# Optimization experiments

Hardware: AMD Instinct MI355X
Metric: run time of the kernel (lower is better)

Reference implementation:

```python
import jax, jax.numpy as jnp
import numpy as np

B, N, C, K = 8, 4096, 128, 16
POOL_RATE = 4  # npoint = N // POOL_RATE


def setup_inputs() -> dict:
    key = jax.random.key(0)
    k1, k2, k3 = jax.random.split(key, 3)
    vertices = jax.random.normal(k1, (B, 3, N), dtype=jnp.float32)
    feature_map = jax.random.normal(k2, (B, C, N), dtype=jnp.float32)
    # pre-flattened global knn indices, values in [0, B*N) as produced upstream
    idx = jax.random.randint(k3, (B * N * K,), 0, B * N, dtype=jnp.int64)
    return {"vertices": vertices, "feature_map": feature_map, "idx": idx}


def farthest_point_sample(xyz, npoint):
    """xyz: (B, N, 3) -> centroid indices (B, npoint).
    Deterministic start at index 0 (torch version uses a random start)."""
    b, n, _ = xyz.shape

    def step(carry, _):
        distance, farthest = carry
        centroid = jnp.take_along_axis(xyz, farthest[:, None, None], axis=1)  # (B,1,3)
        dist = jnp.sum((xyz - centroid) ** 2, axis=-1)  # (B,N)
        distance = jnp.minimum(distance, dist)
        new_farthest = jnp.argmax(distance, axis=-1)
        return (distance, new_farthest), farthest

    dist0 = jnp.full((b, n), 1e10, dtype=xyz.dtype)
    far0 = jnp.zeros((b,), dtype=jnp.int32)
    _, cents = jax.lax.scan(step, (dist0, far0), None, length=npoint)
    return cents.T  # (B, npoint)


def reference(vertices, feature_map, idx):
    b, c, n = feature_map.shape
    # get_graph_feature with precomputed flat idx: gather neighbors then max-pool
    flat = feature_map.transpose(0, 2, 1).reshape(b * n, c)        # (B*N, C)
    neigh = flat[idx].reshape(b, n, K, c)                          # (B,N,K,C)
    pooled = jnp.max(neigh, axis=2)                                # (B,N,C) == (B,C,N) pooled_feature, channel-last

    npoint = n // POOL_RATE
    xyz = vertices.transpose(0, 2, 1)                              # (B,N,3)
    cents = farthest_point_sample(xyz, npoint)                     # (B,npoint)

    vertices_pool = jnp.take_along_axis(xyz, cents[:, :, None], axis=1).transpose(0, 2, 1)     # (B,3,npoint)
    feature_map_pool = jnp.take_along_axis(pooled, cents[:, :, None], axis=1).transpose(0, 2, 1)  # (B,C,npoint)
    return (vertices_pool, feature_map_pool)
```

## Files before the change

### kernel.cpp

```cpp
#include <hip/hip_runtime.h>
#include <hip/hip_bf16.h>
#include <math.h>

#define B_SZ 8
#define N_SZ 4096
#define C_SZ 128
#define K_SZ 16
#define NPOINT 1024

#define FPS_T 256
#define FPS_PAIRS 8

typedef float vf2 __attribute__((ext_vector_type(2)));

template <int CTRL>
__device__ __forceinline__ float dpp_fmax(float x) {
    int t = __builtin_amdgcn_update_dpp(0, __float_as_int(x), CTRL, 0xF, 0xF, true);
    return fmaxf(x, __int_as_float(t));
}
__device__ __forceinline__ float wave_fmax63(float x) {
    x = dpp_fmax<0x111>(x);
    x = dpp_fmax<0x112>(x);
    x = dpp_fmax<0x114>(x);
    x = dpp_fmax<0x118>(x);
    x = dpp_fmax<0x142>(x);
    x = dpp_fmax<0x143>(x);
    return x;
}
__device__ __forceinline__ unsigned long long kmax2(unsigned long long a,
                                                   unsigned long long b) {
    return a > b ? a : b;
}

__global__ void transpose_fm(const float* __restrict__ fm, float* __restrict__ fmT) {
    __shared__ float tile[32][33];
    const int b  = blockIdx.z;
    const int c0 = blockIdx.y * 32;
    const int n0 = blockIdx.x * 32;
    const int tx = threadIdx.x;
    const int ty = threadIdx.y;
    const float* p = fm + (size_t)b * C_SZ * N_SZ;
#pragma unroll
    for (int i = 0; i < 4; i++) {
        tile[ty + i * 8][tx] = p[(size_t)(c0 + ty + i * 8) * N_SZ + n0 + tx];
    }
    __syncthreads();
    float* q = fmT + (size_t)b * N_SZ * C_SZ;
#pragma unroll
    for (int i = 0; i < 4; i++) {
        q[(size_t)(n0 + ty + i * 8) * C_SZ + c0 + tx] = tile[tx][ty + i * 8];
    }
}

__global__ __launch_bounds__(FPS_T) void fps_kernel(
        const float* __restrict__ verts,
        float* __restrict__ out_vp,
        int* __restrict__ cents)
{
#pragma clang fp contract(off)
#pragma clang fp reassociate(off)
    __shared__ float4 sp[N_SZ];
    __shared__ int    scent[NPOINT];
    __shared__ alignas(16) unsigned long long ckey[2][4];

    const int b    = blockIdx.x;
    const int tid  = threadIdx.x;
    const int lane = tid & 63;
    const int wid  = tid >> 6;
    const float* vb = verts + (size_t)b * 3 * N_SZ;

    for (int n = tid; n < N_SZ; n += FPS_T) {
        sp[n] = make_float4(vb[n], vb[N_SZ + n], vb[2 * N_SZ + n], 0.0f);
    }

    const float4* vx4 = (const float4*)vb;
    const float4* vy4 = (const float4*)(vb + N_SZ);
    const float4* vz4 = (const float4*)(vb + 2 * N_SZ);
    vf2 px[FPS_PAIRS], py[FPS_PAIRS], pz[FPS_PAIRS], dd[FPS_PAIRS];
#pragma unroll
    for (int k = 0; k < 4; k++) {
        const float4 x = vx4[tid * 4 + k];
        const float4 y = vy4[tid * 4 + k];
        const float4 z = vz4[tid * 4 + k];
        px[2 * k] = (vf2){x.x, x.y}; px[2 * k + 1] = (vf2){x.z, x.w};
        py[2 * k] = (vf2){y.x, y.y}; py[2 * k + 1] = (vf2){y.z, y.w};
        pz[2 * k] = (vf2){z.x, z.y}; pz[2 * k + 1] = (vf2){z.z, z.w};
        dd[2 * k]     = (vf2){1e10f, 1e10f};
        dd[2 * k + 1] = (vf2){1e10f, 1e10f};
    }
    __syncthreads();

    int ci = 0;
    const float4 c0 = sp[0];
    float cx = c0.x, cy = c0.y, cz = c0.z;

    for (int i = 0; i < NPOINT; i++) {
        if (tid == 0) scent[i] = ci;

        const vf2 cx2 = (vf2){cx, cx};
        const vf2 cy2 = (vf2){cy, cy};
        const vf2 cz2 = (vf2){cz, cz};

        float m = -1.0f;
#pragma unroll
        for (int p = 0; p < FPS_PAIRS; p++) {
            const vf2 dx = px[p] - cx2;
            const vf2 dy = py[p] - cy2;
            const vf2 dz = pz[p] - cz2;
            vf2 s = dx * dx + dy * dy;
            s = s + dz * dz;
            vf2 d;
            d.x = fminf(dd[p].x, s.x);
            d.y = fminf(dd[p].y, s.y);
            dd[p] = d;
            m = fmaxf(m, fmaxf(d.x, d.y));
        }
        const float bv = m;

        int bj = 0;
#pragma unroll
        for (int j = 15; j >= 0; j--) {
            const float v = (j & 1) ? dd[j >> 1].y : dd[j >> 1].x;
            if (v == bv) bj = j;
        }
        const int bn = (tid << 4) | bj;

        const float wm = wave_fmax63(bv);
        const float wmax = __int_as_float(
            __builtin_amdgcn_readlane(__float_as_int(wm), 63));
        const unsigned long long mask = __ballot(bv == wmax);
        const int first = __ffsll(mask) - 1;
        const unsigned nw = (unsigned)__builtin_amdgcn_readlane(bn, first);

        const unsigned long long wkey =
            ((unsigned long long)__float_as_uint(wmax) << 32) |
            (unsigned long long)(4095u - nw);

        const int par = i & 1;
        if (lane == 0) ckey[par][wid] = wkey;
        __syncthreads();

        const ulonglong2* kb = (const ulonglong2*)(&ckey[par][0]);
        const ulonglong2 k01 = kb[0], k23 = kb[1];
        const unsigned long long kk =
            kmax2(kmax2(k01.x, k01.y), kmax2(k23.x, k23.y));

        ci = (int)(4095u - (unsigned)kk);
        const float4 c = sp[ci];
        cx = c.x; cy = c.y; cz = c.z;
    }
    __syncthreads();

    for (int i = tid; i < NPOINT; i += FPS_T) {
        const int cc = scent[i];
        const float4 v = sp[cc];
        cents[b * NPOINT + i] = cc;
        out_vp[(b * 3 + 0) * NPOINT + i] = v.x;
        out_vp[(b * 3 + 1) * NPOINT + i] = v.y;
        out_vp[(b * 3 + 2) * NPOINT + i] = v.z;
    }
}

#define GT_J 16
__global__ __launch_bounds__(1024) void pool_gather_t(
        const float* __restrict__ fmT,
        const int* __restrict__ idx,
        const int* __restrict__ cents,
        float* __restrict__ out_fp)
{
    __shared__ float tile[C_SZ][GT_J + 1];
    const int tid  = threadIdx.x;
    const int lane = tid & 63;
    const int w    = tid >> 6;
    const int j0   = blockIdx.x * GT_J;
    const int gp   = j0 + w;
    const int b    = gp >> 10;
    const int ci   = cents[gp];
    const int* ip  = idx + ((size_t)(b * N_SZ + ci)) * K_SZ;
    const float2* src = (const float2*)fmT;

    float2 acc = make_float2(-INFINITY, -INFINITY);
#pragma unroll
    for (int k = 0; k < K_SZ; k++) {
        const int p = ip[k];
        const float2 v = src[(size_t)p * (C_SZ / 2) + lane];
        acc.x = fmaxf(acc.x, v.x);
        acc.y = fmaxf(acc.y, v.y);
    }
    tile[2 * lane][w]     = acc.x;
    tile[2 * lane + 1][w] = acc.y;
    __syncthreads();

    float* q = out_fp + (size_t)b * C_SZ * NPOINT + (j0 & (NPOINT - 1));
#pragma unroll
    for (int it = 0; it < 2; it++) {
        const int e  = tid + it * 1024;
        const int c  = e >> 4;
        const int jj = e & (GT_J - 1);
        q[(size_t)c * NPOINT + jj] = tile[c][jj];
    }
}

extern "C" void kernel_launch(void* const* d_in, const int* in_sizes, int n_in,
                              void* d_out, int out_size, void* d_ws, size_t ws_size,
                              hipStream_t stream) {
    const float* verts = (const float*)d_in[0];
    const float* fm    = (const float*)d_in[1];
    const int*   idx   = (const int*)d_in[2];

    float* out    = (float*)d_out;
    float* out_vp = out;
    float* out_fp = out + (size_t)B_SZ * 3 * NPOINT;

    char* ws = (char*)d_ws;
    float* fmT   = (float*)ws;
    int*   cents = (int*)(ws + (size_t)B_SZ * N_SZ * C_SZ * 4);

    dim3 tb(32, 8);
    transpose_fm<<<dim3(N_SZ / 32, C_SZ / 32, B_SZ), tb, 0, stream>>>(fm, fmT);
    fps_kernel<<<B_SZ, FPS_T, 0, stream>>>(verts, out_vp, cents);
    pool_gather_t<<<(B_SZ * NPOINT) / GT_J, 1024, 0, stream>>>(fmT, idx, cents, out_fp);
}
```

Baseline: 612.1 us.

## Fuse feature transpose into FPS kernel launch to overlap with serial FPS

```diff
diff --git a/kernel.cpp b/kernel.cpp
--- a/kernel.cpp
+++ b/kernel.cpp
@@ -10,6 +10,9 @@
 
 #define FPS_T 256
 #define FPS_PAIRS 8
+
+#define TR_BLOCKS 512
+#define TR_TILES  8
 
 typedef float vf2 __attribute__((ext_vector_type(2)));
 
@@ -32,28 +35,10 @@
     return a > b ? a : b;
 }
 
-__global__ void transpose_fm(const float* __restrict__ fm, float* __restrict__ fmT) {
-    __shared__ float tile[32][33];
-    const int b  = blockIdx.z;
-    const int c0 = blockIdx.y * 32;
-    const int n0 = blockIdx.x * 32;
-    const int tx = threadIdx.x;
-    const int ty = threadIdx.y;
-    const float* p = fm + (size_t)b * C_SZ * N_SZ;
-#pragma unroll
-    for (int i = 0; i < 4; i++) {
-        tile[ty + i * 8][tx] = p[(size_t)(c0 + ty + i * 8) * N_SZ + n0 + tx];
-    }
-    __syncthreads();
-    float* q = fmT + (size_t)b * N_SZ * C_SZ;
-#pragma unroll
-    for (int i = 0; i < 4; i++) {
-        q[(size_t)(n0 + ty + i * 8) * C_SZ + c0 + tx] = tile[tx][ty + i * 8];
-    }
-}
-
-__global__ __launch_bounds__(FPS_T) void fps_kernel(
+__global__ __launch_bounds__(FPS_T) void fps_fused(
         const float* __restrict__ verts,
+        const float* __restrict__ fm,
+        float* __restrict__ fmT,
         float* __restrict__ out_vp,
         int* __restrict__ cents)
 {
@@ -62,9 +47,41 @@
     __shared__ float4 sp[N_SZ];
     __shared__ int    scent[NPOINT];
     __shared__ alignas(16) unsigned long long ckey[2][4];
+    __shared__ float  trtile[2][32 * 33];
+    __shared__ float  lds_pad[2048];
+
+    const int tid = threadIdx.x;
+
+    if (blockIdx.x >= B_SZ) {
+        const int tx = tid & 31;
+        const int ty = tid >> 5;
+        if (tid == 0xFFFF) lds_pad[0] = 1.0f;
+        for (int tt = 0; tt < TR_TILES; tt++) {
+            const int g  = (blockIdx.x - B_SZ) * TR_TILES + tt;
+            const int b  = g >> 9;
+            const int r  = g & 511;
+            const int n0 = (r & 127) * 32;
+            const int c0 = (r >> 7) * 32;
+            float* tl = trtile[tt & 1];
+            const float* p = fm + (size_t)b * C_SZ * N_SZ;
+#pragma unroll
+            for (int i = 0; i < 4; i++) {
+                tl[(ty + i * 8) * 33 + tx] =
+                    p[(size_t)(c0 + ty + i * 8) * N_SZ + n0 + tx];
+            }
+            __syncthreads();
+            float* q = fmT + (size_t)b * N_SZ * C_SZ;
+#pragma unroll
+            for (int i = 0; i < 4; i++) {
+                q[(size_t)(n0 + ty + i * 8) * C_SZ + c0 + tx] =
+                    tl[tx * 33 + ty + i * 8];
+            }
+            __syncthreads();
+        }
+        return;
+    }
 
     const int b    = blockIdx.x;
-    const int tid  = threadIdx.x;
     const int lane = tid & 63;
     const int wid  = tid >> 6;
     const float* vb = verts + (size_t)b * 3 * N_SZ;
@@ -216,8 +233,6 @@
     float* fmT   = (float*)ws;
     int*   cents = (int*)(ws + (size_t)B_SZ * N_SZ * C_SZ * 4);
 
-    dim3 tb(32, 8);
-    transpose_fm<<<dim3(N_SZ / 32, C_SZ / 32, B_SZ), tb, 0, stream>>>(fm, fmT);
-    fps_kernel<<<B_SZ, FPS_T, 0, stream>>>(verts, out_vp, cents);
+    fps_fused<<<B_SZ + TR_BLOCKS, FPS_T, 0, stream>>>(verts, fm, fmT, out_vp, cents);
     pool_gather_t<<<(B_SZ * NPOINT) / GT_J, 1024, 0, stream>>>(fmT, idx, cents, out_fp);
 }
```

After: 624.4 us. +2.0%, slower.

## Drop transpose; pool per channel from LDS-resident feature slice

Applied to the files above, without the earlier changes.

```diff
diff --git a/kernel.cpp b/kernel.cpp
--- a/kernel.cpp
+++ b/kernel.cpp
@@ -30,26 +30,6 @@
 __device__ __forceinline__ unsigned long long kmax2(unsigned long long a,
                                                    unsigned long long b) {
     return a > b ? a : b;
-}
-
-__global__ void transpose_fm(const float* __restrict__ fm, float* __restrict__ fmT) {
-    __shared__ float tile[32][33];
-    const int b  = blockIdx.z;
-    const int c0 = blockIdx.y * 32;
-    const int n0 = blockIdx.x * 32;
-    const int tx = threadIdx.x;
-    const int ty = threadIdx.y;
-    const float* p = fm + (size_t)b * C_SZ * N_SZ;
-#pragma unroll
-    for (int i = 0; i < 4; i++) {
-        tile[ty + i * 8][tx] = p[(size_t)(c0 + ty + i * 8) * N_SZ + n0 + tx];
-    }
-    __syncthreads();
-    float* q = fmT + (size_t)b * N_SZ * C_SZ;
-#pragma unroll
-    for (int i = 0; i < 4; i++) {
-        q[(size_t)(n0 + ty + i * 8) * C_SZ + c0 + tx] = tile[tx][ty + i * 8];
-    }
 }
 
 __global__ __launch_bounds__(FPS_T) void fps_kernel(
@@ -161,43 +141,44 @@
     }
 }
 
-#define GT_J 16
-__global__ __launch_bounds__(1024) void pool_gather_t(
-        const float* __restrict__ fmT,
+#define PD_T 1024
+__global__ __launch_bounds__(PD_T) void pool_direct(
+        const float* __restrict__ fm,
         const int* __restrict__ idx,
         const int* __restrict__ cents,
         float* __restrict__ out_fp)
 {
-    __shared__ float tile[C_SZ][GT_J + 1];
-    const int tid  = threadIdx.x;
-    const int lane = tid & 63;
-    const int w    = tid >> 6;
-    const int j0   = blockIdx.x * GT_J;
-    const int gp   = j0 + w;
-    const int b    = gp >> 10;
-    const int ci   = cents[gp];
-    const int* ip  = idx + ((size_t)(b * N_SZ + ci)) * K_SZ;
-    const float2* src = (const float2*)fmT;
-
-    float2 acc = make_float2(-INFINITY, -INFINITY);
-#pragma unroll
-    for (int k = 0; k < K_SZ; k++) {
-        const int p = ip[k];
-        const float2 v = src[(size_t)p * (C_SZ / 2) + lane];
-        acc.x = fmaxf(acc.x, v.x);
-        acc.y = fmaxf(acc.y, v.y);
-    }
-    tile[2 * lane][w]     = acc.x;
-    tile[2 * lane + 1][w] = acc.y;
+    __shared__ float sf[B_SZ * N_SZ];
+    const int c   = blockIdx.x;
+    const int tid = threadIdx.x;
+
+    const float4* src4 = (const float4*)fm;
+    float4* sf4 = (float4*)sf;
+#pragma unroll
+    for (int it = 0; it < (B_SZ * N_SZ / 4) / PD_T; it++) {
+        const int ch = it * PD_T + tid;
+        const int b  = ch >> 10;
+        const int n4 = ch & 1023;
+        sf4[ch] = src4[(size_t)(b * C_SZ + c) * (N_SZ / 4) + n4];
+    }
     __syncthreads();
 
-    float* q = out_fp + (size_t)b * C_SZ * NPOINT + (j0 & (NPOINT - 1));
-#pragma unroll
-    for (int it = 0; it < 2; it++) {
-        const int e  = tid + it * 1024;
-        const int c  = e >> 4;
-        const int jj = e & (GT_J - 1);
-        q[(size_t)c * NPOINT + jj] = tile[c][jj];
+#pragma unroll
+    for (int it = 0; it < (B_SZ * NPOINT) / PD_T; it++) {
+        const int gp = it * PD_T + tid;
+        const int b  = gp >> 10;
+        const int ci = cents[gp];
+        const int4* ip = (const int4*)(idx + ((size_t)(b * N_SZ + ci)) * K_SZ);
+        float acc = -INFINITY;
+#pragma unroll
+        for (int q = 0; q < 4; q++) {
+            const int4 p4 = ip[q];
+            acc = fmaxf(acc, sf[p4.x]);
+            acc = fmaxf(acc, sf[p4.y]);
+            acc = fmaxf(acc, sf[p4.z]);
+            acc = fmaxf(acc, sf[p4.w]);
+        }
+        out_fp[(size_t)(b * C_SZ + c) * NPOINT + (gp & (NPOINT - 1))] = acc;
     }
 }
 
@@ -212,12 +193,8 @@
     float* out_vp = out;
     float* out_fp = out + (size_t)B_SZ * 3 * NPOINT;
 
-    char* ws = (char*)d_ws;
-    float* fmT   = (float*)ws;
-    int*   cents = (int*)(ws + (size_t)B_SZ * N_SZ * C_SZ * 4);
-
-    dim3 tb(32, 8);
-    transpose_fm<<<dim3(N_SZ / 32, C_SZ / 32, B_SZ), tb, 0, stream>>>(fm, fmT);
+    int* cents = (int*)d_ws;
+
     fps_kernel<<<B_SZ, FPS_T, 0, stream>>>(verts, out_vp, cents);
-    pool_gather_t<<<(B_SZ * NPOINT) / GT_J, 1024, 0, stream>>>(fmT, idx, cents, out_fp);
-}
+    pool_direct<<<C_SZ, PD_T, 0, stream>>>(fm, idx, cents, out_fp);
+}
```

New measurement: 614.9 us. About the same (+0.5%).
